# Performance work log

Hardware: AMD Instinct MI355X
Metric: run time of the kernel (lower is better)

The kernel has to match this reference:

```python
import jax, jax.numpy as jnp
import numpy as np

N, T, F_IN, F_OUT, E = 20000, 4, 64, 64, 640000


def setup_inputs() -> dict:
    key = jax.random.key(0)
    k1, k2, k3, k4, k5, k6 = jax.random.split(key, 6)
    node_features = jax.random.normal(k1, (N, T, F_IN), dtype=jnp.float32)
    edge_weights = jax.random.uniform(k2, (T, E), dtype=jnp.float32)
    src = jax.random.randint(k3, (E,), 0, N, dtype=jnp.int32)
    dst = jax.random.randint(k4, (E,), 0, N, dtype=jnp.int32)
    W = jax.random.normal(k5, (F_OUT, F_IN), dtype=jnp.float32) / np.sqrt(F_IN)
    b = jax.random.normal(k6, (F_OUT,), dtype=jnp.float32) * 0.01
    return {"node_features": node_features, "edge_weights": edge_weights,
            "src": src, "dst": dst, "W": W, "b": b}


def reference(node_features, edge_weights, src, dst, W, b):
    # u_mul_e: gather source node features and scale by per-edge, per-time weight
    # edge_weights (T, E) -> transposed (E, T) -> broadcast over feature dim
    msg = node_features[src] * edge_weights.T[:, :, None]          # (E, T, F_IN)
    # fn.sum: scatter-sum messages into destination nodes
    h = jax.ops.segment_sum(msg, dst, num_segments=node_features.shape[0])  # (N, T, F_IN)
    # nn.Linear(in_features, out_features)
    return h @ W.T + b                                             # (N, T, F_OUT)
```

## Files before the change

### kernel.cpp

```cpp
#include <hip/hip_runtime.h>

#define N_NODES 20000
#define T_STEPS 4
#define F_DIM   64
#define E_EDGES 640000
#define ROWS    (N_NODES * T_STEPS)
#define ROW_ELEMS (T_STEPS * F_DIM)

#define SCATTER_BLOCKS   (E_EDGES / 1024)
#define TRANSFORM_BLOCKS (ROWS / 64)
#define OVF_CAP          4096

__device__ __forceinline__ unsigned short f32_to_bf16_rne(float f) {
    unsigned u = __float_as_uint(f);
    u += 0x7FFFu + ((u >> 16) & 1u);
    return (unsigned short)(u >> 16);
}
__device__ __forceinline__ float bf16_to_f32(unsigned short h) {
    return __uint_as_float((unsigned)h << 16);
}

__global__ __launch_bounds__(256) void fused_build_kernel(
    const float* __restrict__ x, const float* __restrict__ W,
    unsigned short* __restrict__ yb,
    const int* __restrict__ src, const int* __restrict__ dst,
    const float* __restrict__ ew,
    int* __restrict__ cnt, int4* __restrict__ buckets, int cap,
    int4* __restrict__ ovf, int* __restrict__ ovf_cnt)
{
    if (blockIdx.x < SCATTER_BLOCKS) {
        const int base = blockIdx.x * 1024 + threadIdx.x;
#pragma unroll
        for (int j = 0; j < 4; ++j) {
            const int e = base + j * 256;
            const int d = dst[e];
            int4 rec;
            rec.x = src[e];
            rec.y = (unsigned)f32_to_bf16_rne(ew[e]) |
                    ((unsigned)f32_to_bf16_rne(ew[E_EDGES + e]) << 16);
            rec.z = (unsigned)f32_to_bf16_rne(ew[2 * E_EDGES + e]) |
                    ((unsigned)f32_to_bf16_rne(ew[3 * E_EDGES + e]) << 16);
            rec.w = d;
            const int pos = atomicAdd(&cnt[d], 1);
            if (pos < cap) {
                buckets[(size_t)d * cap + pos] = rec;
            } else {
                const int o = atomicAdd(ovf_cnt, 1);
                if (o < OVF_CAP) ovf[o] = rec;
            }
        }
        return;
    }

    __shared__ float xs[64 * 68];
    __shared__ float wt[64 * 68];
    const int tid  = threadIdx.x;
    const int row0 = (blockIdx.x - SCATTER_BLOCKS) * 64;

    {
        const int o  = tid & 63;
        const int fb = (tid >> 6) * 16;
#pragma unroll
        for (int k = 0; k < 16; ++k) {
            const int f = fb + k;
            wt[f * 68 + o] = W[o * 64 + f];
        }
    }
    {
        const float4* xg = (const float4*)(x + (size_t)row0 * 64);
#pragma unroll
        for (int k = 0; k < 4; ++k) {
            const int q  = k * 256 + tid;
            const int r  = q >> 4;
            const int c4 = (q & 15) * 4;
            *(float4*)&xs[r * 68 + c4] = xg[q];
        }
    }
    __syncthreads();

    const int rg = tid >> 4;
    const int oq = (tid & 15) * 4;

    float acc[4][4];
#pragma unroll
    for (int i = 0; i < 4; ++i)
#pragma unroll
        for (int j = 0; j < 4; ++j) acc[i][j] = 0.0f;

    for (int f = 0; f < 64; ++f) {
        const float4 w4 = *(const float4*)&wt[f * 68 + oq];
#pragma unroll
        for (int i = 0; i < 4; ++i) {
            const float xv = xs[(rg * 4 + i) * 68 + f];
            acc[i][0] += xv * w4.x;
            acc[i][1] += xv * w4.y;
            acc[i][2] += xv * w4.z;
            acc[i][3] += xv * w4.w;
        }
    }

#pragma unroll
    for (int i = 0; i < 4; ++i) {
        const int r = row0 + rg * 4 + i;
        ushort4 h;
        h.x = f32_to_bf16_rne(acc[i][0]);
        h.y = f32_to_bf16_rne(acc[i][1]);
        h.z = f32_to_bf16_rne(acc[i][2]);
        h.w = f32_to_bf16_rne(acc[i][3]);
        *(ushort4*)(yb + (size_t)r * 64 + oq) = h;
    }
}

__global__ __launch_bounds__(256) void accumulate_kernel(
    const unsigned short* __restrict__ yb, const int* __restrict__ cnt,
    const int4* __restrict__ buckets, int cap,
    const float* __restrict__ b, float* __restrict__ out)
{
    const int lane = threadIdx.x & 63;
    const int n    = blockIdx.x * 4 + (threadIdx.x >> 6);
    const int t    = lane >> 4;
    const int l4   = lane * 4;

    int deg = cnt[n];
    if (deg > cap) deg = cap;
    const int4* rp = buckets + (size_t)n * cap;

    float4 acc = make_float4(0.f, 0.f, 0.f, 0.f);

    int k = 0;
    for (; k + 8 <= deg; k += 8) {
        int4 r[8];
#pragma unroll
        for (int i = 0; i < 8; ++i) r[i] = rp[k + i];
        ushort4 v[8];
#pragma unroll
        for (int i = 0; i < 8; ++i)
            v[i] = *(const ushort4*)(yb + (size_t)r[i].x * ROW_ELEMS + l4);
#pragma unroll
        for (int i = 0; i < 8; ++i) {
            const unsigned word = (t & 2) ? (unsigned)r[i].z : (unsigned)r[i].y;
            const float w = bf16_to_f32((t & 1) ? (unsigned short)(word >> 16)
                                                : (unsigned short)(word & 0xFFFF));
            acc.x += bf16_to_f32(v[i].x) * w;
            acc.y += bf16_to_f32(v[i].y) * w;
            acc.z += bf16_to_f32(v[i].z) * w;
            acc.w += bf16_to_f32(v[i].w) * w;
        }
    }
    if (k + 4 <= deg) {
        int4 r[4];
#pragma unroll
        for (int i = 0; i < 4; ++i) r[i] = rp[k + i];
        ushort4 v[4];
#pragma unroll
        for (int i = 0; i < 4; ++i)
            v[i] = *(const ushort4*)(yb + (size_t)r[i].x * ROW_ELEMS + l4);
#pragma unroll
        for (int i = 0; i < 4; ++i) {
            const unsigned word = (t & 2) ? (unsigned)r[i].z : (unsigned)r[i].y;
            const float w = bf16_to_f32((t & 1) ? (unsigned short)(word >> 16)
                                                : (unsigned short)(word & 0xFFFF));
            acc.x += bf16_to_f32(v[i].x) * w;
            acc.y += bf16_to_f32(v[i].y) * w;
            acc.z += bf16_to_f32(v[i].z) * w;
            acc.w += bf16_to_f32(v[i].w) * w;
        }
        k += 4;
    }
    for (; k < deg; ++k) {
        const int4 r = rp[k];
        const unsigned word = (t & 2) ? (unsigned)r.z : (unsigned)r.y;
        const float w = bf16_to_f32((t & 1) ? (unsigned short)(word >> 16)
                                            : (unsigned short)(word & 0xFFFF));
        const ushort4 v = *(const ushort4*)(yb + (size_t)r.x * ROW_ELEMS + l4);
        acc.x += bf16_to_f32(v.x) * w;
        acc.y += bf16_to_f32(v.y) * w;
        acc.z += bf16_to_f32(v.z) * w;
        acc.w += bf16_to_f32(v.w) * w;
    }

    const float4 bv = *(const float4*)(b + (lane & 15) * 4);
    acc.x += bv.x; acc.y += bv.y; acc.z += bv.z; acc.w += bv.w;
    *(float4*)(out + (size_t)n * ROW_ELEMS + l4) = acc;
}

__global__ __launch_bounds__(256) void overflow_kernel(
    const unsigned short* __restrict__ yb, const int4* __restrict__ ovf,
    const int* __restrict__ ovf_cnt, float* __restrict__ out)
{
    const int lane = threadIdx.x & 63;
    const int w_id = threadIdx.x >> 6;
    const int t    = lane >> 4;
    const int l4   = lane * 4;
    int m = *ovf_cnt;
    if (m > OVF_CAP) m = OVF_CAP;
    for (int i = w_id; i < m; i += 4) {
        const int4 r = ovf[i];
        const unsigned word = (t & 2) ? (unsigned)r.z : (unsigned)r.y;
        const float w = bf16_to_f32((t & 1) ? (unsigned short)(word >> 16)
                                            : (unsigned short)(word & 0xFFFF));
        const ushort4 v = *(const ushort4*)(yb + (size_t)r.x * ROW_ELEMS + l4);
        float* op = out + (size_t)r.w * ROW_ELEMS + l4;
        atomicAdd(op + 0, bf16_to_f32(v.x) * w);
        atomicAdd(op + 1, bf16_to_f32(v.y) * w);
        atomicAdd(op + 2, bf16_to_f32(v.z) * w);
        atomicAdd(op + 3, bf16_to_f32(v.w) * w);
    }
}

extern "C" void kernel_launch(void* const* d_in, const int* in_sizes, int n_in,
                              void* d_out, int out_size, void* d_ws, size_t ws_size,
                              hipStream_t stream) {
    const float* x   = (const float*)d_in[0];
    const float* ew  = (const float*)d_in[1];
    const int*   src = (const int*)  d_in[2];
    const int*   dst = (const int*)  d_in[3];
    const float* W   = (const float*)d_in[4];
    const float* b   = (const float*)d_in[5];
    float*       out = (float*)d_out;

    char* ws = (char*)d_ws;
    size_t off = 0;
    auto alloc = [&](size_t bytes) {
        void* p = ws + off;
        off += (bytes + 255) & ~(size_t)255;
        return p;
    };
    unsigned short* yb  = (unsigned short*)alloc((size_t)ROWS * 64 * 2);
    int*            cnt = (int*) alloc((N_NODES + 1) * sizeof(int));
    int4*           ovf = (int4*)alloc((size_t)OVF_CAP * sizeof(int4));
    int*            ovf_cnt = cnt + N_NODES;

    size_t rem = (ws_size > off) ? (ws_size - off) : 0;
    int cap = (int)(rem / ((size_t)N_NODES * sizeof(int4)));
    if (cap > 128) cap = 128;
    if (cap < 1) cap = 1;
    int4* buckets = (int4*)(ws + off);

    hipMemsetAsync(cnt, 0, (N_NODES + 1) * sizeof(int), stream);
    fused_build_kernel<<<SCATTER_BLOCKS + TRANSFORM_BLOCKS, 256, 0, stream>>>(
        x, W, yb, src, dst, ew, cnt, buckets, cap, ovf, ovf_cnt);
    accumulate_kernel<<<N_NODES / 4, 256, 0, stream>>>(
        yb, cnt, buckets, cap, b, out);
    overflow_kernel<<<1, 256, 0, stream>>>(yb, ovf, ovf_cnt, out);
}
```

Baseline: 175.8 us.

## Store edge indices in buckets and fold overflow handling into accumulate

```diff
diff --git a/kernel.cpp b/kernel.cpp
--- a/kernel.cpp
+++ b/kernel.cpp
@@ -23,30 +23,29 @@
 __global__ __launch_bounds__(256) void fused_build_kernel(
     const float* __restrict__ x, const float* __restrict__ W,
     unsigned short* __restrict__ yb,
-    const int* __restrict__ src, const int* __restrict__ dst,
-    const float* __restrict__ ew,
-    int* __restrict__ cnt, int4* __restrict__ buckets, int cap,
-    int4* __restrict__ ovf, int* __restrict__ ovf_cnt)
+    const int* __restrict__ dst, const float* __restrict__ ew,
+    int* __restrict__ cnt, int* __restrict__ buckets, int cap,
+    uint2* __restrict__ wpk,
+    int* __restrict__ ovf, int* __restrict__ ovf_cnt)
 {
     if (blockIdx.x < SCATTER_BLOCKS) {
         const int base = blockIdx.x * 1024 + threadIdx.x;
 #pragma unroll
         for (int j = 0; j < 4; ++j) {
             const int e = base + j * 256;
+            uint2 wv;
+            wv.x = (unsigned)f32_to_bf16_rne(ew[e]) |
+                   ((unsigned)f32_to_bf16_rne(ew[E_EDGES + e]) << 16);
+            wv.y = (unsigned)f32_to_bf16_rne(ew[2 * E_EDGES + e]) |
+                   ((unsigned)f32_to_bf16_rne(ew[3 * E_EDGES + e]) << 16);
+            wpk[e] = wv;
             const int d = dst[e];
-            int4 rec;
-            rec.x = src[e];
-            rec.y = (unsigned)f32_to_bf16_rne(ew[e]) |
-                    ((unsigned)f32_to_bf16_rne(ew[E_EDGES + e]) << 16);
-            rec.z = (unsigned)f32_to_bf16_rne(ew[2 * E_EDGES + e]) |
-                    ((unsigned)f32_to_bf16_rne(ew[3 * E_EDGES + e]) << 16);
-            rec.w = d;
             const int pos = atomicAdd(&cnt[d], 1);
             if (pos < cap) {
-                buckets[(size_t)d * cap + pos] = rec;
+                __builtin_nontemporal_store(e, &buckets[(size_t)d * cap + pos]);
             } else {
                 const int o = atomicAdd(ovf_cnt, 1);
-                if (o < OVF_CAP) ovf[o] = rec;
+                if (o < OVF_CAP) ovf[o] = e;
             }
         }
         return;
@@ -113,7 +112,10 @@
 
 __global__ __launch_bounds__(256) void accumulate_kernel(
     const unsigned short* __restrict__ yb, const int* __restrict__ cnt,
-    const int4* __restrict__ buckets, int cap,
+    const int* __restrict__ buckets, int cap,
+    const int* __restrict__ src, const uint2* __restrict__ wpk,
+    const int* __restrict__ dstg,
+    const int* __restrict__ ovf, const int* __restrict__ ovf_cnt,
     const float* __restrict__ b, float* __restrict__ out)
 {
     const int lane = threadIdx.x & 63;
@@ -123,22 +125,28 @@
 
     int deg = cnt[n];
     if (deg > cap) deg = cap;
-    const int4* rp = buckets + (size_t)n * cap;
+    const int* rp = buckets + (size_t)n * cap;
 
     float4 acc = make_float4(0.f, 0.f, 0.f, 0.f);
 
     int k = 0;
     for (; k + 8 <= deg; k += 8) {
-        int4 r[8];
-#pragma unroll
-        for (int i = 0; i < 8; ++i) r[i] = rp[k + i];
+        int e[8];
+#pragma unroll
+        for (int i = 0; i < 8; ++i) e[i] = rp[k + i];
+        int s[8];
+        uint2 w2[8];
+#pragma unroll
+        for (int i = 0; i < 8; ++i) s[i] = src[e[i]];
+#pragma unroll
+        for (int i = 0; i < 8; ++i) w2[i] = wpk[e[i]];
         ushort4 v[8];
 #pragma unroll
         for (int i = 0; i < 8; ++i)
-            v[i] = *(const ushort4*)(yb + (size_t)r[i].x * ROW_ELEMS + l4);
+            v[i] = *(const ushort4*)(yb + (size_t)s[i] * ROW_ELEMS + l4);
 #pragma unroll
         for (int i = 0; i < 8; ++i) {
-            const unsigned word = (t & 2) ? (unsigned)r[i].z : (unsigned)r[i].y;
+            const unsigned word = (t & 2) ? w2[i].y : w2[i].x;
             const float w = bf16_to_f32((t & 1) ? (unsigned short)(word >> 16)
                                                 : (unsigned short)(word & 0xFFFF));
             acc.x += bf16_to_f32(v[i].x) * w;
@@ -148,16 +156,22 @@
         }
     }
     if (k + 4 <= deg) {
-        int4 r[4];
-#pragma unroll
-        for (int i = 0; i < 4; ++i) r[i] = rp[k + i];
+        int e[4];
+#pragma unroll
+        for (int i = 0; i < 4; ++i) e[i] = rp[k + i];
+        int s[4];
+        uint2 w2[4];
+#pragma unroll
+        for (int i = 0; i < 4; ++i) s[i] = src[e[i]];
+#pragma unroll
+        for (int i = 0; i < 4; ++i) w2[i] = wpk[e[i]];
         ushort4 v[4];
 #pragma unroll
         for (int i = 0; i < 4; ++i)
-            v[i] = *(const ushort4*)(yb + (size_t)r[i].x * ROW_ELEMS + l4);
+            v[i] = *(const ushort4*)(yb + (size_t)s[i] * ROW_ELEMS + l4);
 #pragma unroll
         for (int i = 0; i < 4; ++i) {
-            const unsigned word = (t & 2) ? (unsigned)r[i].z : (unsigned)r[i].y;
+            const unsigned word = (t & 2) ? w2[i].y : w2[i].x;
             const float w = bf16_to_f32((t & 1) ? (unsigned short)(word >> 16)
                                                 : (unsigned short)(word & 0xFFFF));
             acc.x += bf16_to_f32(v[i].x) * w;
@@ -168,44 +182,42 @@
         k += 4;
     }
     for (; k < deg; ++k) {
-        const int4 r = rp[k];
-        const unsigned word = (t & 2) ? (unsigned)r.z : (unsigned)r.y;
+        const int e = rp[k];
+        const int s0 = src[e];
+        const uint2 ww = wpk[e];
+        const unsigned word = (t & 2) ? ww.y : ww.x;
         const float w = bf16_to_f32((t & 1) ? (unsigned short)(word >> 16)
                                             : (unsigned short)(word & 0xFFFF));
-        const ushort4 v = *(const ushort4*)(yb + (size_t)r.x * ROW_ELEMS + l4);
+        const ushort4 v = *(const ushort4*)(yb + (size_t)s0 * ROW_ELEMS + l4);
         acc.x += bf16_to_f32(v.x) * w;
         acc.y += bf16_to_f32(v.y) * w;
         acc.z += bf16_to_f32(v.z) * w;
         acc.w += bf16_to_f32(v.w) * w;
     }
 
+    {
+        int m = *ovf_cnt;
+        if (m > OVF_CAP) m = OVF_CAP;
+        for (int i = 0; i < m; ++i) {
+            const int e = ovf[i];
+            if (dstg[e] == n) {
+                const int s0 = src[e];
+                const uint2 ww = wpk[e];
+                const unsigned word = (t & 2) ? ww.y : ww.x;
+                const float w = bf16_to_f32((t & 1) ? (unsigned short)(word >> 16)
+                                                    : (unsigned short)(word & 0xFFFF));
+                const ushort4 v = *(const ushort4*)(yb + (size_t)s0 * ROW_ELEMS + l4);
+                acc.x += bf16_to_f32(v.x) * w;
+                acc.y += bf16_to_f32(v.y) * w;
+                acc.z += bf16_to_f32(v.z) * w;
+                acc.w += bf16_to_f32(v.w) * w;
+            }
+        }
+    }
+
     const float4 bv = *(const float4*)(b + (lane & 15) * 4);
     acc.x += bv.x; acc.y += bv.y; acc.z += bv.z; acc.w += bv.w;
     *(float4*)(out + (size_t)n * ROW_ELEMS + l4) = acc;
-}
-
-__global__ __launch_bounds__(256) void overflow_kernel(
-    const unsigned short* __restrict__ yb, const int4* __restrict__ ovf,
-    const int* __restrict__ ovf_cnt, float* __restrict__ out)
-{
-    const int lane = threadIdx.x & 63;
-    const int w_id = threadIdx.x >> 6;
-    const int t    = lane >> 4;
-    const int l4   = lane * 4;
-    int m = *ovf_cnt;
-    if (m > OVF_CAP) m = OVF_CAP;
-    for (int i = w_id; i < m; i += 4) {
-        const int4 r = ovf[i];
-        const unsigned word = (t & 2) ? (unsigned)r.z : (unsigned)r.y;
-        const float w = bf16_to_f32((t & 1) ? (unsigned short)(word >> 16)
-                                            : (unsigned short)(word & 0xFFFF));
-        const ushort4 v = *(const ushort4*)(yb + (size_t)r.x * ROW_ELEMS + l4);
-        float* op = out + (size_t)r.w * ROW_ELEMS + l4;
-        atomicAdd(op + 0, bf16_to_f32(v.x) * w);
-        atomicAdd(op + 1, bf16_to_f32(v.y) * w);
-        atomicAdd(op + 2, bf16_to_f32(v.z) * w);
-        atomicAdd(op + 3, bf16_to_f32(v.w) * w);
-    }
 }
 
 extern "C" void kernel_launch(void* const* d_in, const int* in_sizes, int n_in,
@@ -228,19 +240,19 @@
     };
     unsigned short* yb  = (unsigned short*)alloc((size_t)ROWS * 64 * 2);
     int*            cnt = (int*) alloc((N_NODES + 1) * sizeof(int));
-    int4*           ovf = (int4*)alloc((size_t)OVF_CAP * sizeof(int4));
+    uint2*          wpk = (uint2*)alloc((size_t)E_EDGES * sizeof(uint2));
+    int*            ovf = (int*) alloc((size_t)OVF_CAP * sizeof(int));
     int*            ovf_cnt = cnt + N_NODES;
 
     size_t rem = (ws_size > off) ? (ws_size - off) : 0;
-    int cap = (int)(rem / ((size_t)N_NODES * sizeof(int4)));
-    if (cap > 128) cap = 128;
+    int cap = (int)(rem / ((size_t)N_NODES * sizeof(int)));
+    if (cap > 64) cap = 64;
     if (cap < 1) cap = 1;
-    int4* buckets = (int4*)(ws + off);
+    int* buckets = (int*)(ws + off);
 
     hipMemsetAsync(cnt, 0, (N_NODES + 1) * sizeof(int), stream);
     fused_build_kernel<<<SCATTER_BLOCKS + TRANSFORM_BLOCKS, 256, 0, stream>>>(
-        x, W, yb, src, dst, ew, cnt, buckets, cap, ovf, ovf_cnt);
+        x, W, yb, dst, ew, cnt, buckets, cap, wpk, ovf, ovf_cnt);
     accumulate_kernel<<<N_NODES / 4, 256, 0, stream>>>(
-        yb, cnt, buckets, cap, b, out);
-    overflow_kernel<<<1, 256, 0, stream>>>(yb, ovf, ovf_cnt, out);
-}
+        yb, cnt, buckets, cap, src, wpk, dst, ovf, ovf_cnt, b, out);
+}
```

Result: slower. 212.6 us (+21.0%).
